# Kernel tuning notes

Measured on AMD Instinct MI355X. Metric: run time of the kernel, lower is better.

Reference implementation:

```python
import jax, jax.numpy as jnp
import numpy as np

L1, L2, B = 512, 512, 2
D1, D2, BN = 256, 256, 256
NEG = jnp.float32(-1e12)


def setup_inputs() -> dict:
    key = jax.random.key(0)
    ks = jax.random.split(key, 8)
    s = 0.05
    return {
        "ctx_1": jax.random.normal(ks[0], (L1, B, D1), jnp.float32),
        "ctx_2": jax.random.normal(ks[1], (L2, B, D2), jnp.float32),
        "ctx_1_mask": jnp.ones((L1, B), jnp.float32),
        "ctx_2_mask": jnp.ones((L2, B), jnp.float32),
        # mlp_hid: Conv2d(D1+D2 -> BN, 1x1) with bias
        "Wh": jax.random.normal(ks[2], (D1 + D2, BN), jnp.float32) * s,
        "bh": jnp.zeros((BN,), jnp.float32),
        # mlp_out: Conv2d(BN -> 1, 1x1), bias=False (mlp_bias default)
        "wo": jax.random.normal(ks[3], (BN,), jnp.float32) * s,
        # project_1_to_2 / project_2_to_1: Linear(D1+D2 -> BN) with bias
        "W12": jax.random.normal(ks[4], (D2 + D1, BN), jnp.float32) * s,
        "b12": jnp.zeros((BN,), jnp.float32),
        "W21": jax.random.normal(ks[5], (D1 + D2, BN), jnp.float32) * s,
        "b21": jnp.zeros((BN,), jnp.float32),
    }


def reference(ctx_1, ctx_2, ctx_1_mask, ctx_2_mask, Wh, bh, wo, W12, b12, W21, b21):
    d1 = ctx_1.shape[-1]
    # 1x1 conv on cat([b_ctx_1, b_ctx_2]) == sum of two independent projections
    Wh1, Wh2 = Wh[:d1], Wh[d1:]
    p1 = jnp.einsum('lbd,dk->blk', ctx_1, Wh1)            # (B, L1, K)
    p2 = jnp.einsum('mbd,dk->bmk', ctx_2, Wh2)            # (B, L2, K)
    hidden = jnp.tanh(p1[:, :, None, :] + p2[:, None, :, :] + bh)  # (B, L1, L2, K)
    affinity = jnp.einsum('blmk,k->blm', hidden, wo)      # (B, L1, L2)
    # masked in both directions
    affinity = affinity + (1.0 - ctx_1_mask.T)[:, :, None] * NEG
    affinity = affinity + (1.0 - ctx_2_mask.T)[:, None, :] * NEG
    # 1 -> 2 direction: softmax over L2
    dist_1_to_2 = jax.nn.softmax(affinity, axis=2)        # (B, L1, L2)
    context_1_to_2 = jnp.einsum('lbd,blm->mbd', ctx_1, dist_1_to_2)  # (L2, B, D1)
    seq_1_to_2 = jnp.tanh(jnp.concatenate([ctx_2, context_1_to_2], axis=-1) @ W12 + b12)
    # 2 -> 1 direction: softmax over L1 (then contracted over L2, as in the torch code)
    dist_2_to_1 = jax.nn.softmax(affinity, axis=1)        # (B, L1, L2)
    context_2_to_1 = jnp.einsum('mbd,blm->lbd', ctx_2, dist_2_to_1)  # (L1, B, D2)
    seq_2_to_1 = jnp.tanh(jnp.concatenate([ctx_1, context_2_to_1], axis=-1) @ W21 + b21)
    return (seq_2_to_1, seq_1_to_2)
```

## Files before the change

### kernel.cpp

```cpp
#include <hip/hip_runtime.h>


#define NEGC (-1e12f)
#define TWO_LOG2E 2.8853900817779268f
#define LOG2E 1.4426950408889634f
#define N2LOG2E (-2.8853900817779268f)

typedef __attribute__((ext_vector_type(8))) short bf16x8;
typedef __attribute__((ext_vector_type(4))) float f32x4;

__device__ __forceinline__ short f2bf(float x)
{
    union { float f; unsigned u; } v; v.f = x;
    unsigned r = (v.u + 0x7FFFu + ((v.u >> 16) & 1u)) >> 16;
    return (short)r;
}

__global__ __launch_bounds__(256) void k_projE(
    const float* __restrict__ ctx1, const float* __restrict__ ctx2,
    const float* __restrict__ Wh, const float* __restrict__ bh,
    const float* __restrict__ mask1, const float* __restrict__ mask2,
    float* __restrict__ E1, float* __restrict__ E2,
    float* __restrict__ p1, float* __restrict__ p2,
    float* __restrict__ S1, float* __restrict__ S2)
{
    const int t  = threadIdx.x;
    const int g  = blockIdx.z;
    const int r0 = blockIdx.x * 32;
    const int n0 = blockIdx.y * 64;

    const float* A    = g ? ctx2       : ctx1;
    const float* W    = g ? Wh + 65536 : Wh;
    const float* bias = g ? 0          : bh;
    float*       outp = g ? E2         : E1;

    if (g == 0 && blockIdx.x == 0 && blockIdx.y == 0) {
        for (int idx = t; idx < 1024; idx += 256) {
            int row = idx >> 1, b = idx & 1;
            p1[b * 512 + row] = __builtin_amdgcn_exp2f(LOG2E * (1.f - mask1[idx]) * NEGC);
            p2[b * 512 + row] = __builtin_amdgcn_exp2f(LOG2E * (1.f - mask2[idx]) * NEGC);
            S1[b * 512 + row] = 0.f;
            S2[b * 512 + row] = 0.f;
        }
    }

    __shared__ __align__(16) short Abf[32 * 264];
    __shared__ __align__(16) short Bbf[64 * 264];

    #pragma unroll
    for (int i = 0; i < 8; ++i) {
        int slot = i * 256 + t;
        int r = slot >> 6, kq = (slot & 63) << 2;
        float4 v = *(const float4*)(A + (r0 + r) * 256 + kq);
        short4 s; s.x = f2bf(v.x); s.y = f2bf(v.y); s.z = f2bf(v.z); s.w = f2bf(v.w);
        *(short4*)(Abf + r * 264 + kq) = s;
    }
    #pragma unroll
    for (int i = 0; i < 16; ++i) {
        int slot = i * 256 + t;
        int bk = slot >> 4, bn4 = (slot & 15) << 2;
        float4 v = *(const float4*)(W + bk * 256 + n0 + bn4);
        Bbf[(bn4 + 0) * 264 + bk] = f2bf(v.x);
        Bbf[(bn4 + 1) * 264 + bk] = f2bf(v.y);
        Bbf[(bn4 + 2) * 264 + bk] = f2bf(v.z);
        Bbf[(bn4 + 3) * 264 + bk] = f2bf(v.w);
    }
    __syncthreads();

    const int w    = t >> 6;
    const int lane = t & 63;
    const int quad = lane >> 4;
    const int lr   = lane & 15;
    const int h    = w & 1;
    const int c    = w >> 1;

    f32x4 acc[2] = {};

    #pragma unroll
    for (int s = 0; s < 8; ++s) {
        const int kb = s * 32 + quad * 8;
        bf16x8 a = *(const bf16x8*)(Abf + (h * 16 + lr) * 264 + kb);
        #pragma unroll
        for (int nc = 0; nc < 2; ++nc) {
            bf16x8 b = *(const bf16x8*)(Bbf + (c * 32 + nc * 16 + lr) * 264 + kb);
            acc[nc] = __builtin_amdgcn_mfma_f32_16x16x32_bf16(a, b, acc[nc], 0, 0, 0);
        }
    }

    #pragma unroll
    for (int nc = 0; nc < 2; ++nc) {
        const int col = n0 + c * 32 + nc * 16 + lr;
        const float bv = bias ? bias[col] : 0.f;
        #pragma unroll
        for (int reg = 0; reg < 4; ++reg) {
            int row  = r0 + h * 16 + quad * 4 + reg;
            int orow = ((row & 1) << 9) + (row >> 1);
            float v = acc[nc][reg] + bv;
            outp[orow * 256 + col] = __builtin_amdgcn_exp2f(v * TWO_LOG2E);
        }
    }
}

#define PAIR(AV, QV, WV, ACC) do {                                    \
    float x0_ = fmaf(AV.x, QV.x, 1.f);                                \
    float x1_ = fmaf(AV.y, QV.y, 1.f);                                \
    float x2_ = fmaf(AV.z, QV.z, 1.f);                                \
    float x3_ = fmaf(AV.w, QV.w, 1.f);                                \
    float r01_ = __builtin_amdgcn_rcpf(x0_ * x1_);                    \
    float r23_ = __builtin_amdgcn_rcpf(x2_ * x3_);                    \
    float z01_ = fmaf(WV.y, x0_, WV.x * x1_);                         \
    float z23_ = fmaf(WV.w, x2_, WV.z * x3_);                         \
    ACC = fmaf(r01_, z01_, ACC);                                      \
    ACC = fmaf(r23_, z23_, ACC);                                      \
} while (0)

__global__ __launch_bounds__(256) void k_mid(
    const float* __restrict__ ctx1, const float* __restrict__ ctx2,
    const float* __restrict__ W12, const float* __restrict__ b12,
    const float* __restrict__ W21, const float* __restrict__ b21,
    const float* __restrict__ E1g, const float* __restrict__ E2g,
    const float* __restrict__ wo,
    const float* __restrict__ p1g, const float* __restrict__ p2g,
    float* __restrict__ P12, float* __restrict__ U1,
    float* __restrict__ P21, float* __restrict__ U2,
    float* __restrict__ EN, float* __restrict__ ET,
    float* __restrict__ S1, float* __restrict__ S2)
{
    __shared__ __align__(16) char smem[38400];

    const int t   = threadIdx.x;
    const int bid = blockIdx.x;
    const int r3  = bid % 3;

    if (r3 == 2) {
        const int idx = bid / 3;
        const int g   = idx >> 6;
        const int r0  = (idx & 15) * 64;
        const int n0  = ((idx >> 4) & 3) * 64;

        const float* A; const float* W; const float* bias; float* outp;
        switch (g) {
          case 0:  A = ctx2; W = W12;         bias = b12; outp = P12; break;
          case 1:  A = ctx1; W = W12 + 65536; bias = 0;   outp = U1;  break;
          case 2:  A = ctx1; W = W21;         bias = b21; outp = P21; break;
          default: A = ctx2; W = W21 + 65536; bias = 0;   outp = U2;  break;
        }

        short* Abf = (short*)smem;
        short* Bbf = Abf + 64 * 136;

        const int w    = t >> 6;
        const int lane = t & 63;
        const int quad = lane >> 4;
        const int lr   = lane & 15;

        f32x4 acc[4] = {};

        for (int kc = 0; kc < 256; kc += 128) {
            #pragma unroll
            for (int i = 0; i < 8; ++i) {
                int slot = i * 256 + t;
                int r = slot >> 5, kq = (slot & 31) << 2;
                float4 v = *(const float4*)(A + (r0 + r) * 256 + kc + kq);
                short4 s; s.x = f2bf(v.x); s.y = f2bf(v.y); s.z = f2bf(v.z); s.w = f2bf(v.w);
                *(short4*)(Abf + r * 136 + kq) = s;
            }
            #pragma unroll
            for (int i = 0; i < 8; ++i) {
                int slot = i * 256 + t;
                int bk = slot >> 4, bn4 = (slot & 15) << 2;
                float4 v = *(const float4*)(W + (kc + bk) * 256 + n0 + bn4);
                Bbf[(bn4 + 0) * 136 + bk] = f2bf(v.x);
                Bbf[(bn4 + 1) * 136 + bk] = f2bf(v.y);
                Bbf[(bn4 + 2) * 136 + bk] = f2bf(v.z);
                Bbf[(bn4 + 3) * 136 + bk] = f2bf(v.w);
            }
            __syncthreads();
            #pragma unroll
            for (int s = 0; s < 4; ++s) {
                const int kb = s * 32 + quad * 8;
                bf16x8 a = *(const bf16x8*)(Abf + (w * 16 + lr) * 136 + kb);
                #pragma unroll
                for (int nc = 0; nc < 4; ++nc) {
                    bf16x8 b = *(const bf16x8*)(Bbf + (nc * 16 + lr) * 136 + kb);
                    acc[nc] = __builtin_amdgcn_mfma_f32_16x16x32_bf16(a, b, acc[nc], 0, 0, 0);
                }
            }
            __syncthreads();
        }

        #pragma unroll
        for (int nc = 0; nc < 4; ++nc) {
            const int col = n0 + nc * 16 + lr;
            const float bv = bias ? bias[col] : 0.f;
            #pragma unroll
            for (int reg = 0; reg < 4; ++reg) {
                int row  = r0 + w * 16 + quad * 4 + reg;
                int orow = ((row & 1) << 9) + (row >> 1);
                outp[orow * 256 + col] = acc[nc][reg] + bv;
            }
        }
    } else {
        const int aidx = (bid / 3) * 2 + r3;
        const int l0 = (aidx & 15) * 32;
        const int m0 = ((aidx >> 4) & 15) * 32;
        const int b  = aidx >> 8;

        float* E1s  = (float*)smem;
        float* E2s  = E1s + 32 * 132;
        float* affs = E2s + 32 * 132;

        const int tl = t >> 4, tm = t & 15;
        float acc[2][2] = {};

        for (int kc = 0; kc < 256; kc += 128) {
            #pragma unroll
            for (int i = 0; i < 4; ++i) {
                int slot = i * 256 + t;
                int r = slot >> 5, kq = (slot & 31) << 2;
                *(float4*)(E1s + r * 132 + kq) =
                    *(const float4*)(E1g + (((b << 9) + l0 + r) << 8) + kc + kq);
                *(float4*)(E2s + r * 132 + kq) =
                    *(const float4*)(E2g + (((b << 9) + m0 + r) << 8) + kc + kq);
            }
            __syncthreads();
            #pragma unroll 4
            for (int k0 = 0; k0 < 128; k0 += 4) {
                const float4 w  = *(const float4*)(wo + kc + k0);
                const float4 a0 = *(const float4*)(E1s + tl * 132 + k0);
                const float4 a1 = *(const float4*)(E1s + (tl + 16) * 132 + k0);
                const float4 q0 = *(const float4*)(E2s + tm * 132 + k0);
                const float4 q1 = *(const float4*)(E2s + (tm + 16) * 132 + k0);
                PAIR(a0, q0, w, acc[0][0]);
                PAIR(a0, q1, w, acc[0][1]);
                PAIR(a1, q0, w, acc[1][0]);
                PAIR(a1, q1, w, acc[1][1]);
            }
            __syncthreads();
        }

        affs[tl * 36 + tm]             = __builtin_amdgcn_exp2f(acc[0][0] * N2LOG2E);
        affs[tl * 36 + tm + 16]        = __builtin_amdgcn_exp2f(acc[0][1] * N2LOG2E);
        affs[(tl + 16) * 36 + tm]      = __builtin_amdgcn_exp2f(acc[1][0] * N2LOG2E);
        affs[(tl + 16) * 36 + tm + 16] = __builtin_amdgcn_exp2f(acc[1][1] * N2LOG2E);
        __syncthreads();

        const int r  = t >> 3;
        const int c4 = (t & 7) << 2;
        {
            float4 e = *(const float4*)(affs + r * 36 + c4);
            const float p1r = p1g[(b << 9) + l0 + r];
            float4 vn = make_float4(e.x * p1r, e.y * p1r, e.z * p1r, e.w * p1r);
            *(float4*)(EN + (((b << 9) + l0 + r) << 9) + m0 + c4) = vn;
            float4 p2v = *(const float4*)(p2g + (b << 9) + m0 + c4);
            float s = (e.x * p2v.x + e.y * p2v.y) + (e.z * p2v.z + e.w * p2v.w);
            s += __shfl_xor(s, 1, 64);
            s += __shfl_xor(s, 2, 64);
            s += __shfl_xor(s, 4, 64);
            if ((t & 7) == 0) atomicAdd(S1 + (b << 9) + l0 + r, s);
        }
        {
            float4 te;
            te.x = affs[(c4 + 0) * 36 + r];
            te.y = affs[(c4 + 1) * 36 + r];
            te.z = affs[(c4 + 2) * 36 + r];
            te.w = affs[(c4 + 3) * 36 + r];
            const float p2r = p2g[(b << 9) + m0 + r];
            float4 vt = make_float4(te.x * p2r, te.y * p2r, te.z * p2r, te.w * p2r);
            *(float4*)(ET + (((b << 9) + m0 + r) << 9) + l0 + c4) = vt;
            float4 p1v = *(const float4*)(p1g + (b << 9) + l0 + c4);
            float s = (te.x * p1v.x + te.y * p1v.y) + (te.z * p1v.z + te.w * p1v.w);
            s += __shfl_xor(s, 1, 64);
            s += __shfl_xor(s, 2, 64);
            s += __shfl_xor(s, 4, 64);
            if ((t & 7) == 0) atomicAdd(S2 + (b << 9) + m0 + r, s);
        }
    }
}

__global__ __launch_bounds__(256) void k_final(
    const float* __restrict__ EN, const float* __restrict__ ET,
    const float* __restrict__ U1, const float* __restrict__ U2,
    const float* __restrict__ P12, const float* __restrict__ P21,
    const float* __restrict__ S1, const float* __restrict__ S2,
    float* __restrict__ out)
{
    const int t   = threadIdx.x;
    const int r0  = blockIdx.x * 32, n0 = blockIdx.y * 32;
    const int dir = blockIdx.z >> 1, b = blockIdx.z & 1;
    const float* Ag = (dir == 0 ? ET  : EN)  + b * 262144;
    const float* Sg = (dir == 0 ? S1  : S2)  + b * 512;
    const float* Bg = (dir == 0 ? U1  : U2)  + b * 131072;
    const float* Pg = (dir == 0 ? P12 : P21) + b * 131072;
    float* o = out + (dir == 0 ? 262144 : 0);

    __shared__ __align__(16) short Abf[32 * 136];
    __shared__ __align__(16) short Bbf[32 * 136];
    __shared__ __align__(16) float rs[512];

    for (int i = t; i < 512; i += 256)
        rs[i] = __builtin_amdgcn_rcpf(Sg[i]);

    const int w    = t >> 6;
    const int lane = t & 63;
    const int quad = lane >> 4;
    const int lr   = lane & 15;
    const int wr   = (w >> 1) << 4, wc = (w & 1) << 4;
    const int col  = n0 + wc + lr;

    float pre[4];
    #pragma unroll
    for (int reg = 0; reg < 4; ++reg) {
        const int m = r0 + wr + quad * 4 + reg;
        pre[reg] = Pg[(m << 8) + col];
    }
    __syncthreads();

    f32x4 acc = {};

    for (int kc = 0; kc < 512; kc += 128) {
        #pragma unroll
        for (int i = 0; i < 4; ++i) {
            int slot = i * 256 + t;
            int r = slot >> 5, kq = (slot & 31) << 2;
            float4 v = *(const float4*)(Ag + ((r0 + r) << 9) + kc + kq);
            const float* rp = rs + kc + kq;
            short4 s;
            s.x = f2bf(v.x * rp[0]); s.y = f2bf(v.y * rp[1]);
            s.z = f2bf(v.z * rp[2]); s.w = f2bf(v.w * rp[3]);
            *(short4*)(Abf + r * 136 + kq) = s;
        }
        #pragma unroll
        for (int i = 0; i < 4; ++i) {
            int slot = i * 256 + t;
            int bk = slot >> 3, bn4 = (slot & 7) << 2;
            float4 v = *(const float4*)(Bg + ((kc + bk) << 8) + n0 + bn4);
            Bbf[(bn4 + 0) * 136 + bk] = f2bf(v.x);
            Bbf[(bn4 + 1) * 136 + bk] = f2bf(v.y);
            Bbf[(bn4 + 2) * 136 + bk] = f2bf(v.z);
            Bbf[(bn4 + 3) * 136 + bk] = f2bf(v.w);
        }
        __syncthreads();
        #pragma unroll
        for (int s = 0; s < 4; ++s) {
            const int kb = s * 32 + quad * 8;
            bf16x8 a  = *(const bf16x8*)(Abf + (wr + lr) * 136 + kb);
            bf16x8 bb = *(const bf16x8*)(Bbf + (wc + lr) * 136 + kb);
            acc = __builtin_amdgcn_mfma_f32_16x16x32_bf16(a, bb, acc, 0, 0, 0);
        }
        __syncthreads();
    }

    #pragma unroll
    for (int reg = 0; reg < 4; ++reg) {
        const int m = r0 + wr + quad * 4 + reg;
        float v = acc[reg] + pre[reg];
        float tv = 1.f - 2.f * __builtin_amdgcn_rcpf(
                       __builtin_amdgcn_exp2f(v * TWO_LOG2E) + 1.f);
        o[((m << 1) + b) * 256 + col] = tv;
    }
}

extern "C" void kernel_launch(void* const* d_in, const int* in_sizes, int n_in,
                              void* d_out, int out_size, void* d_ws, size_t ws_size,
                              hipStream_t stream)
{
    const float* ctx1 = (const float*)d_in[0];
    const float* ctx2 = (const float*)d_in[1];
    const float* m1   = (const float*)d_in[2];
    const float* m2   = (const float*)d_in[3];
    const float* Wh   = (const float*)d_in[4];
    const float* bh   = (const float*)d_in[5];
    const float* wo   = (const float*)d_in[6];
    const float* W12  = (const float*)d_in[7];
    const float* b12  = (const float*)d_in[8];
    const float* W21  = (const float*)d_in[9];
    const float* b21  = (const float*)d_in[10];
    float* out = (float*)d_out;
    float* ws  = (float*)d_ws;

    float* E1  = ws;
    float* E2  = E1  + 262144;
    float* P12 = E2  + 262144;
    float* U1  = P12 + 262144;
    float* P21 = U1  + 262144;
    float* U2  = P21 + 262144;
    float* p1  = U2  + 262144;
    float* p2  = p1  + 1024;
    float* S1  = p2  + 1024;
    float* S2  = S1  + 1024;
    float* EN  = S2  + 1024;
    float* ET  = EN  + 524288;

    hipLaunchKernelGGL(k_projE, dim3(32, 4, 2), dim3(256), 0, stream,
                       ctx1, ctx2, Wh, bh, m1, m2, E1, E2, p1, p2, S1, S2);
    hipLaunchKernelGGL(k_mid, dim3(768, 1, 1), dim3(256), 0, stream,
                       ctx1, ctx2, W12, b12, W21, b21,
                       E1, E2, wo, p1, p2,
                       P12, U1, P21, U2, EN, ET, S1, S2);
    hipLaunchKernelGGL(k_final, dim3(16, 8, 4), dim3(256), 0, stream,
                       EN, ET, U1, U2, P12, P21, S1, S2, out);
}
```

Before: 115.3 us.

## Regroup kernels: fuse all projections, split affinity into its own full-K kernel

Moves the W12/W21 projection GEMMs out of the mid kernel and runs them alongside the Wh projection in one launch. The affinity computation becomes a dedicated kernel that stages the full K=256 of E1/E2 in shared memory in a single pass, which removes one sync round. Its inner loop uses packed v_pk_fma_f32 via inline asm, and bf16 conversion now goes through the native __bf16 cast. The aim is to balance work across launches and cut per-block overhead, at the cost of higher LDS use per affinity block (about 71KB), which lowers occupancy.

After: 118.7 us. +3.0%, slower.

```diff
diff --git a/kernel.cpp b/kernel.cpp
--- a/kernel.cpp
+++ b/kernel.cpp
@@ -8,135 +8,120 @@
 
 typedef __attribute__((ext_vector_type(8))) short bf16x8;
 typedef __attribute__((ext_vector_type(4))) float f32x4;
+typedef __attribute__((ext_vector_type(2))) float f32x2;
 
 __device__ __forceinline__ short f2bf(float x)
 {
-    union { float f; unsigned u; } v; v.f = x;
-    unsigned r = (v.u + 0x7FFFu + ((v.u >> 16) & 1u)) >> 16;
-    return (short)r;
-}
-
-__global__ __launch_bounds__(256) void k_projE(
+    return __builtin_bit_cast(short, (__bf16)x);
+}
+
+__device__ __forceinline__ f32x2 pk_fma(f32x2 a, f32x2 b, f32x2 c)
+{
+    f32x2 d;
+    asm("v_pk_fma_f32 %0, %1, %2, %3" : "=v"(d) : "v"(a), "v"(b), "v"(c));
+    return d;
+}
+
+__global__ __launch_bounds__(256) void k_proj(
     const float* __restrict__ ctx1, const float* __restrict__ ctx2,
     const float* __restrict__ Wh, const float* __restrict__ bh,
+    const float* __restrict__ W12, const float* __restrict__ b12,
+    const float* __restrict__ W21, const float* __restrict__ b21,
     const float* __restrict__ mask1, const float* __restrict__ mask2,
     float* __restrict__ E1, float* __restrict__ E2,
+    float* __restrict__ P12, float* __restrict__ U1,
+    float* __restrict__ P21, float* __restrict__ U2,
     float* __restrict__ p1, float* __restrict__ p2,
     float* __restrict__ S1, float* __restrict__ S2)
 {
-    const int t  = threadIdx.x;
-    const int g  = blockIdx.z;
-    const int r0 = blockIdx.x * 32;
-    const int n0 = blockIdx.y * 64;
-
-    const float* A    = g ? ctx2       : ctx1;
-    const float* W    = g ? Wh + 65536 : Wh;
-    const float* bias = g ? 0          : bh;
-    float*       outp = g ? E2         : E1;
-
-    if (g == 0 && blockIdx.x == 0 && blockIdx.y == 0) {
-        for (int idx = t; idx < 1024; idx += 256) {
-            int row = idx >> 1, b = idx & 1;
-            p1[b * 512 + row] = __builtin_amdgcn_exp2f(LOG2E * (1.f - mask1[idx]) * NEGC);
-            p2[b * 512 + row] = __builtin_amdgcn_exp2f(LOG2E * (1.f - mask2[idx]) * NEGC);
-            S1[b * 512 + row] = 0.f;
-            S2[b * 512 + row] = 0.f;
-        }
-    }
-
-    __shared__ __align__(16) short Abf[32 * 264];
-    __shared__ __align__(16) short Bbf[64 * 264];
-
-    #pragma unroll
-    for (int i = 0; i < 8; ++i) {
-        int slot = i * 256 + t;
-        int r = slot >> 6, kq = (slot & 63) << 2;
-        float4 v = *(const float4*)(A + (r0 + r) * 256 + kq);
-        short4 s; s.x = f2bf(v.x); s.y = f2bf(v.y); s.z = f2bf(v.z); s.w = f2bf(v.w);
-        *(short4*)(Abf + r * 264 + kq) = s;
-    }
-    #pragma unroll
-    for (int i = 0; i < 16; ++i) {
-        int slot = i * 256 + t;
-        int bk = slot >> 4, bn4 = (slot & 15) << 2;
-        float4 v = *(const float4*)(W + bk * 256 + n0 + bn4);
-        Bbf[(bn4 + 0) * 264 + bk] = f2bf(v.x);
-        Bbf[(bn4 + 1) * 264 + bk] = f2bf(v.y);
-        Bbf[(bn4 + 2) * 264 + bk] = f2bf(v.z);
-        Bbf[(bn4 + 3) * 264 + bk] = f2bf(v.w);
-    }
-    __syncthreads();
+    __shared__ __align__(16) char smem[50688];
+
+    const int t    = threadIdx.x;
+    const int bid  = blockIdx.x;
+    const int path = bid & 1;
+    const int idx  = bid >> 1;
 
     const int w    = t >> 6;
     const int lane = t & 63;
     const int quad = lane >> 4;
     const int lr   = lane & 15;
-    const int h    = w & 1;
-    const int c    = w >> 1;
-
-    f32x4 acc[2] = {};
-
-    #pragma unroll
-    for (int s = 0; s < 8; ++s) {
-        const int kb = s * 32 + quad * 8;
-        bf16x8 a = *(const bf16x8*)(Abf + (h * 16 + lr) * 264 + kb);
+
+    if (bid == 0) {
+        for (int i = t; i < 1024; i += 256) {
+            int row = i >> 1, b = i & 1;
+            p1[b * 512 + row] = __builtin_amdgcn_exp2f(LOG2E * (1.f - mask1[i]) * NEGC);
+            p2[b * 512 + row] = __builtin_amdgcn_exp2f(LOG2E * (1.f - mask2[i]) * NEGC);
+            S1[b * 512 + row] = 0.f;
+            S2[b * 512 + row] = 0.f;
+        }
+    }
+
+    if (path == 0) {
+        const int g  = idx >> 7;
+        const int i7 = idx & 127;
+        const int r0 = (i7 & 31) * 32;
+        const int n0 = (i7 >> 5) * 64;
+
+        const float* A    = g ? ctx2       : ctx1;
+        const float* W    = g ? Wh + 65536 : Wh;
+        const float* bias = g ? 0          : bh;
+        float*       outp = g ? E2         : E1;
+
+        short* Abf = (short*)smem;
+        short* Bbf = Abf + 32 * 264;
+
+        #pragma unroll
+        for (int i = 0; i < 8; ++i) {
+            int slot = i * 256 + t;
+            int r = slot >> 6, kq = (slot & 63) << 2;
+            float4 v = *(const float4*)(A + (r0 + r) * 256 + kq);
+            short4 s; s.x = f2bf(v.x); s.y = f2bf(v.y); s.z = f2bf(v.z); s.w = f2bf(v.w);
+            *(short4*)(Abf + r * 264 + kq) = s;
+        }
+        #pragma unroll
+        for (int i = 0; i < 16; ++i) {
+            int slot = i * 256 + t;
+            int bk = slot >> 4, bn4 = (slot & 15) << 2;
+            float4 v = *(const float4*)(W + bk * 256 + n0 + bn4);
+            Bbf[(bn4 + 0) * 264 + bk] = f2bf(v.x);
+            Bbf[(bn4 + 1) * 264 + bk] = f2bf(v.y);
+            Bbf[(bn4 + 2) * 264 + bk] = f2bf(v.z);
+            Bbf[(bn4 + 3) * 264 + bk] = f2bf(v.w);
+        }
+        __syncthreads();
+
+        const int h = w & 1;
+        const int c = w >> 1;
+
+        f32x4 acc[2] = {};
+
+        #pragma unroll
+        for (int s = 0; s < 8; ++s) {
+            const int kb = s * 32 + quad * 8;
+            bf16x8 a = *(const bf16x8*)(Abf + (h * 16 + lr) * 264 + kb);
+            #pragma unroll
+            for (int nc = 0; nc < 2; ++nc) {
+                bf16x8 b = *(const bf16x8*)(Bbf + (c * 32 + nc * 16 + lr) * 264 + kb);
+                acc[nc] = __builtin_amdgcn_mfma_f32_16x16x32_bf16(a, b, acc[nc], 0, 0, 0);
+            }
+        }
+
         #pragma unroll
         for (int nc = 0; nc < 2; ++nc) {
-            bf16x8 b = *(const bf16x8*)(Bbf + (c * 32 + nc * 16 + lr) * 264 + kb);
-            acc[nc] = __builtin_amdgcn_mfma_f32_16x16x32_bf16(a, b, acc[nc], 0, 0, 0);
-        }
-    }
-
-    #pragma unroll
-    for (int nc = 0; nc < 2; ++nc) {
-        const int col = n0 + c * 32 + nc * 16 + lr;
-        const float bv = bias ? bias[col] : 0.f;
-        #pragma unroll
-        for (int reg = 0; reg < 4; ++reg) {
-            int row  = r0 + h * 16 + quad * 4 + reg;
-            int orow = ((row & 1) << 9) + (row >> 1);
-            float v = acc[nc][reg] + bv;
-            outp[orow * 256 + col] = __builtin_amdgcn_exp2f(v * TWO_LOG2E);
-        }
-    }
-}
-
-#define PAIR(AV, QV, WV, ACC) do {                                    \
-    float x0_ = fmaf(AV.x, QV.x, 1.f);                                \
-    float x1_ = fmaf(AV.y, QV.y, 1.f);                                \
-    float x2_ = fmaf(AV.z, QV.z, 1.f);                                \
-    float x3_ = fmaf(AV.w, QV.w, 1.f);                                \
-    float r01_ = __builtin_amdgcn_rcpf(x0_ * x1_);                    \
-    float r23_ = __builtin_amdgcn_rcpf(x2_ * x3_);                    \
-    float z01_ = fmaf(WV.y, x0_, WV.x * x1_);                         \
-    float z23_ = fmaf(WV.w, x2_, WV.z * x3_);                         \
-    ACC = fmaf(r01_, z01_, ACC);                                      \
-    ACC = fmaf(r23_, z23_, ACC);                                      \
-} while (0)
-
-__global__ __launch_bounds__(256) void k_mid(
-    const float* __restrict__ ctx1, const float* __restrict__ ctx2,
-    const float* __restrict__ W12, const float* __restrict__ b12,
-    const float* __restrict__ W21, const float* __restrict__ b21,
-    const float* __restrict__ E1g, const float* __restrict__ E2g,
-    const float* __restrict__ wo,
-    const float* __restrict__ p1g, const float* __restrict__ p2g,
-    float* __restrict__ P12, float* __restrict__ U1,
-    float* __restrict__ P21, float* __restrict__ U2,
-    float* __restrict__ EN, float* __restrict__ ET,
-    float* __restrict__ S1, float* __restrict__ S2)
-{
-    __shared__ __align__(16) char smem[38400];
-
-    const int t   = threadIdx.x;
-    const int bid = blockIdx.x;
-    const int r3  = bid % 3;
-
-    if (r3 == 2) {
-        const int idx = bid / 3;
-        const int g   = idx >> 6;
-        const int r0  = (idx & 15) * 64;
-        const int n0  = ((idx >> 4) & 3) * 64;
+            const int col = n0 + c * 32 + nc * 16 + lr;
+            const float bv = bias ? bias[col] : 0.f;
+            #pragma unroll
+            for (int reg = 0; reg < 4; ++reg) {
+                int row  = r0 + h * 16 + quad * 4 + reg;
+                int orow = ((row & 1) << 9) + (row >> 1);
+                float v = acc[nc][reg] + bv;
+                outp[orow * 256 + col] = __builtin_amdgcn_exp2f(v * TWO_LOG2E);
+            }
+        }
+    } else {
+        const int g  = idx >> 6;
+        const int r0 = (idx & 15) * 64;
+        const int n0 = ((idx >> 4) & 3) * 64;
 
         const float* A; const float* W; const float* bias; float* outp;
         switch (g) {
@@ -148,11 +133,6 @@
 
         short* Abf = (short*)smem;
         short* Bbf = Abf + 64 * 136;
-
-        const int w    = t >> 6;
-        const int lane = t & 63;
-        const int quad = lane >> 4;
-        const int lr   = lane & 15;
 
         f32x4 acc[4] = {};
 
@@ -200,81 +180,106 @@
                 outp[orow * 256 + col] = acc[nc][reg] + bv;
             }
         }
-    } else {
-        const int aidx = (bid / 3) * 2 + r3;
-        const int l0 = (aidx & 15) * 32;
-        const int m0 = ((aidx >> 4) & 15) * 32;
-        const int b  = aidx >> 8;
-
-        float* E1s  = (float*)smem;
-        float* E2s  = E1s + 32 * 132;
-        float* affs = E2s + 32 * 132;
-
-        const int tl = t >> 4, tm = t & 15;
-        float acc[2][2] = {};
-
-        for (int kc = 0; kc < 256; kc += 128) {
-            #pragma unroll
-            for (int i = 0; i < 4; ++i) {
-                int slot = i * 256 + t;
-                int r = slot >> 5, kq = (slot & 31) << 2;
-                *(float4*)(E1s + r * 132 + kq) =
-                    *(const float4*)(E1g + (((b << 9) + l0 + r) << 8) + kc + kq);
-                *(float4*)(E2s + r * 132 + kq) =
-                    *(const float4*)(E2g + (((b << 9) + m0 + r) << 8) + kc + kq);
-            }
-            __syncthreads();
-            #pragma unroll 4
-            for (int k0 = 0; k0 < 128; k0 += 4) {
-                const float4 w  = *(const float4*)(wo + kc + k0);
-                const float4 a0 = *(const float4*)(E1s + tl * 132 + k0);
-                const float4 a1 = *(const float4*)(E1s + (tl + 16) * 132 + k0);
-                const float4 q0 = *(const float4*)(E2s + tm * 132 + k0);
-                const float4 q1 = *(const float4*)(E2s + (tm + 16) * 132 + k0);
-                PAIR(a0, q0, w, acc[0][0]);
-                PAIR(a0, q1, w, acc[0][1]);
-                PAIR(a1, q0, w, acc[1][0]);
-                PAIR(a1, q1, w, acc[1][1]);
-            }
-            __syncthreads();
-        }
-
-        affs[tl * 36 + tm]             = __builtin_amdgcn_exp2f(acc[0][0] * N2LOG2E);
-        affs[tl * 36 + tm + 16]        = __builtin_amdgcn_exp2f(acc[0][1] * N2LOG2E);
-        affs[(tl + 16) * 36 + tm]      = __builtin_amdgcn_exp2f(acc[1][0] * N2LOG2E);
-        affs[(tl + 16) * 36 + tm + 16] = __builtin_amdgcn_exp2f(acc[1][1] * N2LOG2E);
-        __syncthreads();
-
-        const int r  = t >> 3;
-        const int c4 = (t & 7) << 2;
-        {
-            float4 e = *(const float4*)(affs + r * 36 + c4);
-            const float p1r = p1g[(b << 9) + l0 + r];
-            float4 vn = make_float4(e.x * p1r, e.y * p1r, e.z * p1r, e.w * p1r);
-            *(float4*)(EN + (((b << 9) + l0 + r) << 9) + m0 + c4) = vn;
-            float4 p2v = *(const float4*)(p2g + (b << 9) + m0 + c4);
-            float s = (e.x * p2v.x + e.y * p2v.y) + (e.z * p2v.z + e.w * p2v.w);
-            s += __shfl_xor(s, 1, 64);
-            s += __shfl_xor(s, 2, 64);
-            s += __shfl_xor(s, 4, 64);
-            if ((t & 7) == 0) atomicAdd(S1 + (b << 9) + l0 + r, s);
-        }
-        {
-            float4 te;
-            te.x = affs[(c4 + 0) * 36 + r];
-            te.y = affs[(c4 + 1) * 36 + r];
-            te.z = affs[(c4 + 2) * 36 + r];
-            te.w = affs[(c4 + 3) * 36 + r];
-            const float p2r = p2g[(b << 9) + m0 + r];
-            float4 vt = make_float4(te.x * p2r, te.y * p2r, te.z * p2r, te.w * p2r);
-            *(float4*)(ET + (((b << 9) + m0 + r) << 9) + l0 + c4) = vt;
-            float4 p1v = *(const float4*)(p1g + (b << 9) + l0 + c4);
-            float s = (te.x * p1v.x + te.y * p1v.y) + (te.z * p1v.z + te.w * p1v.w);
-            s += __shfl_xor(s, 1, 64);
-            s += __shfl_xor(s, 2, 64);
-            s += __shfl_xor(s, 4, 64);
-            if ((t & 7) == 0) atomicAdd(S2 + (b << 9) + m0 + r, s);
-        }
+    }
+}
+
+__device__ __forceinline__ void pair4(const float4 AV, const float4 QV,
+                                      const float4 WV, const f32x2 one,
+                                      float& ACC)
+{
+    f32x2 alo = {AV.x, AV.y}, ahi = {AV.z, AV.w};
+    f32x2 qlo = {QV.x, QV.y}, qhi = {QV.z, QV.w};
+    f32x2 x01 = pk_fma(alo, qlo, one);
+    f32x2 x23 = pk_fma(ahi, qhi, one);
+    float r01 = __builtin_amdgcn_rcpf(x01.x * x01.y);
+    float r23 = __builtin_amdgcn_rcpf(x23.x * x23.y);
+    float z01 = fmaf(WV.y, x01.x, WV.x * x01.y);
+    float z23 = fmaf(WV.w, x23.x, WV.z * x23.y);
+    ACC = fmaf(r01, z01, ACC);
+    ACC = fmaf(r23, z23, ACC);
+}
+
+__global__ __launch_bounds__(256) void k_aff(
+    const float* __restrict__ E1g, const float* __restrict__ E2g,
+    const float* __restrict__ wo,
+    const float* __restrict__ p1g, const float* __restrict__ p2g,
+    float* __restrict__ EN, float* __restrict__ ET,
+    float* __restrict__ S1, float* __restrict__ S2)
+{
+    const int t   = threadIdx.x;
+    const int bid = blockIdx.x;
+    const int l0 = (bid & 15) * 32;
+    const int m0 = ((bid >> 4) & 15) * 32;
+    const int b  = bid >> 8;
+
+    __shared__ __align__(16) float E1s[32 * 260];
+    __shared__ __align__(16) float E2s[32 * 260];
+    __shared__ __align__(16) float affs[32 * 36];
+
+    #pragma unroll
+    for (int i = 0; i < 8; ++i) {
+        int slot = i * 256 + t;
+        int r = slot >> 6, kq = (slot & 63) << 2;
+        *(float4*)(E1s + r * 260 + kq) =
+            *(const float4*)(E1g + (((b << 9) + l0 + r) << 8) + kq);
+        *(float4*)(E2s + r * 260 + kq) =
+            *(const float4*)(E2g + (((b << 9) + m0 + r) << 8) + kq);
+    }
+    __syncthreads();
+
+    const int tl = t >> 4, tm = t & 15;
+    float acc[2][2] = {};
+    const f32x2 one = {1.f, 1.f};
+
+    #pragma unroll 4
+    for (int k0 = 0; k0 < 256; k0 += 4) {
+        const float4 w  = *(const float4*)(wo + k0);
+        const float4 a0 = *(const float4*)(E1s + tl * 260 + k0);
+        const float4 a1 = *(const float4*)(E1s + (tl + 16) * 260 + k0);
+        const float4 q0 = *(const float4*)(E2s + tm * 260 + k0);
+        const float4 q1 = *(const float4*)(E2s + (tm + 16) * 260 + k0);
+        pair4(a0, q0, w, one, acc[0][0]);
+        pair4(a0, q1, w, one, acc[0][1]);
+        pair4(a1, q0, w, one, acc[1][0]);
+        pair4(a1, q1, w, one, acc[1][1]);
+    }
+    __syncthreads();
+
+    affs[tl * 36 + tm]             = __builtin_amdgcn_exp2f(acc[0][0] * N2LOG2E);
+    affs[tl * 36 + tm + 16]        = __builtin_amdgcn_exp2f(acc[0][1] * N2LOG2E);
+    affs[(tl + 16) * 36 + tm]      = __builtin_amdgcn_exp2f(acc[1][0] * N2LOG2E);
+    affs[(tl + 16) * 36 + tm + 16] = __builtin_amdgcn_exp2f(acc[1][1] * N2LOG2E);
+    __syncthreads();
+
+    const int r  = t >> 3;
+    const int c4 = (t & 7) << 2;
+    {
+        float4 e = *(const float4*)(affs + r * 36 + c4);
+        const float p1r = p1g[(b << 9) + l0 + r];
+        float4 vn = make_float4(e.x * p1r, e.y * p1r, e.z * p1r, e.w * p1r);
+        *(float4*)(EN + (((b << 9) + l0 + r) << 9) + m0 + c4) = vn;
+        float4 p2v = *(const float4*)(p2g + (b << 9) + m0 + c4);
+        float s = (e.x * p2v.x + e.y * p2v.y) + (e.z * p2v.z + e.w * p2v.w);
+        s += __shfl_xor(s, 1, 64);
+        s += __shfl_xor(s, 2, 64);
+        s += __shfl_xor(s, 4, 64);
+        if ((t & 7) == 0) atomicAdd(S1 + (b << 9) + l0 + r, s);
+    }
+    {
+        float4 te;
+        te.x = affs[(c4 + 0) * 36 + r];
+        te.y = affs[(c4 + 1) * 36 + r];
+        te.z = affs[(c4 + 2) * 36 + r];
+        te.w = affs[(c4 + 3) * 36 + r];
+        const float p2r = p2g[(b << 9) + m0 + r];
+        float4 vt = make_float4(te.x * p2r, te.y * p2r, te.z * p2r, te.w * p2r);
+        *(float4*)(ET + (((b << 9) + m0 + r) << 9) + l0 + c4) = vt;
+        float4 p1v = *(const float4*)(p1g + (b << 9) + l0 + c4);
+        float s = (te.x * p1v.x + te.y * p1v.y) + (te.z * p1v.z + te.w * p1v.w);
+        s += __shfl_xor(s, 1, 64);
+        s += __shfl_xor(s, 2, 64);
+        s += __shfl_xor(s, 4, 64);
+        if ((t & 7) == 0) atomicAdd(S2 + (b << 9) + m0 + r, s);
     }
 }
 
@@ -323,11 +328,11 @@
         for (int i = 0; i < 4; ++i) {
             int slot = i * 256 + t;
             int r = slot >> 5, kq = (slot & 31) << 2;
-            float4 v = *(const float4*)(Ag + ((r0 + r) << 9) + kc + kq);
-            const float* rp = rs + kc + kq;
+            float4 v  = *(const float4*)(Ag + ((r0 + r) << 9) + kc + kq);
+            float4 rv = *(const float4*)(rs + kc + kq);
             short4 s;
-            s.x = f2bf(v.x * rp[0]); s.y = f2bf(v.y * rp[1]);
-            s.z = f2bf(v.z * rp[2]); s.w = f2bf(v.w * rp[3]);
+            s.x = f2bf(v.x * rv.x); s.y = f2bf(v.y * rv.y);
+            s.z = f2bf(v.z * rv.z); s.w = f2bf(v.w * rv.w);
             *(short4*)(Abf + r * 136 + kq) = s;
         }
         #pragma unroll
@@ -392,12 +397,11 @@
     float* EN  = S2  + 1024;
     float* ET  = EN  + 524288;
 
-    hipLaunchKernelGGL(k_projE, dim3(32, 4, 2), dim3(256), 0, stream,
-                       ctx1, ctx2, Wh, bh, m1, m2, E1, E2, p1, p2, S1, S2);
-    hipLaunchKernelGGL(k_mid, dim3(768, 1, 1), dim3(256), 0, stream,
-                       ctx1, ctx2, W12, b12, W21, b21,
-                       E1, E2, wo, p1, p2,
-                       P12, U1, P21, U2, EN, ET, S1, S2);
+    hipLaunchKernelGGL(k_proj, dim3(512, 1, 1), dim3(256), 0, stream,
+                       ctx1, ctx2, Wh, bh, W12, b12, W21, b21, m1, m2,
+                       E1, E2, P12, U1, P21, U2, p1, p2, S1, S2);
+    hipLaunchKernelGGL(k_aff, dim3(512, 1, 1), dim3(256), 0, stream,
+                       E1, E2, wo, p1, p2, EN, ET, S1, S2);
     hipLaunchKernelGGL(k_final, dim3(16, 8, 4), dim3(256), 0, stream,
                        EN, ET, U1, U2, P12, P21, S1, S2, out);
 }
```

## Store affinity matrices as bf16 and fold softmax normalizer into B operand

Applied to the files above, without the earlier changes.

The mid kernel now writes the scaled affinity matrices EN/ET as bf16 rather than fp32, which halves the intermediate write and read traffic between kernels. The final kernel copies these bf16 tiles directly into shared memory with 16-byte loads. The per-k reciprocal softmax normalizer is now applied to the B operand (U1/U2) during its conversion, since the scale runs along the shared k dimension. The bf16 conversion now uses the compiler's native __bf16 cast. Risk: the normalization is now applied after bf16 rounding of the A values instead of before, which slightly changes rounding.

After: 113.3 us. Within noise of the previous version (-1.7%).

```diff
diff --git a/kernel.cpp b/kernel.cpp
--- a/kernel.cpp
+++ b/kernel.cpp
@@ -11,9 +11,7 @@
 
 __device__ __forceinline__ short f2bf(float x)
 {
-    union { float f; unsigned u; } v; v.f = x;
-    unsigned r = (v.u + 0x7FFFu + ((v.u >> 16) & 1u)) >> 16;
-    return (short)r;
+    return __builtin_bit_cast(short, (__bf16)x);
 }
 
 __global__ __launch_bounds__(256) void k_projE(
@@ -123,7 +121,7 @@
     const float* __restrict__ p1g, const float* __restrict__ p2g,
     float* __restrict__ P12, float* __restrict__ U1,
     float* __restrict__ P21, float* __restrict__ U2,
-    float* __restrict__ EN, float* __restrict__ ET,
+    short* __restrict__ EN, short* __restrict__ ET,
     float* __restrict__ S1, float* __restrict__ S2)
 {
     __shared__ __align__(16) char smem[38400];
@@ -250,8 +248,10 @@
         {
             float4 e = *(const float4*)(affs + r * 36 + c4);
             const float p1r = p1g[(b << 9) + l0 + r];
-            float4 vn = make_float4(e.x * p1r, e.y * p1r, e.z * p1r, e.w * p1r);
-            *(float4*)(EN + (((b << 9) + l0 + r) << 9) + m0 + c4) = vn;
+            short4 vn;
+            vn.x = f2bf(e.x * p1r); vn.y = f2bf(e.y * p1r);
+            vn.z = f2bf(e.z * p1r); vn.w = f2bf(e.w * p1r);
+            *(short4*)(EN + (((b << 9) + l0 + r) << 9) + m0 + c4) = vn;
             float4 p2v = *(const float4*)(p2g + (b << 9) + m0 + c4);
             float s = (e.x * p2v.x + e.y * p2v.y) + (e.z * p2v.z + e.w * p2v.w);
             s += __shfl_xor(s, 1, 64);
@@ -266,8 +266,10 @@
             te.z = affs[(c4 + 2) * 36 + r];
             te.w = affs[(c4 + 3) * 36 + r];
             const float p2r = p2g[(b << 9) + m0 + r];
-            float4 vt = make_float4(te.x * p2r, te.y * p2r, te.z * p2r, te.w * p2r);
-            *(float4*)(ET + (((b << 9) + m0 + r) << 9) + l0 + c4) = vt;
+            short4 vt;
+            vt.x = f2bf(te.x * p2r); vt.y = f2bf(te.y * p2r);
+            vt.z = f2bf(te.z * p2r); vt.w = f2bf(te.w * p2r);
+            *(short4*)(ET + (((b << 9) + m0 + r) << 9) + l0 + c4) = vt;
             float4 p1v = *(const float4*)(p1g + (b << 9) + l0 + c4);
             float s = (te.x * p1v.x + te.y * p1v.y) + (te.z * p1v.z + te.w * p1v.w);
             s += __shfl_xor(s, 1, 64);
@@ -279,7 +281,7 @@
 }
 
 __global__ __launch_bounds__(256) void k_final(
-    const float* __restrict__ EN, const float* __restrict__ ET,
+    const short* __restrict__ EN, const short* __restrict__ ET,
     const float* __restrict__ U1, const float* __restrict__ U2,
     const float* __restrict__ P12, const float* __restrict__ P21,
     const float* __restrict__ S1, const float* __restrict__ S2,
@@ -288,7 +290,7 @@
     const int t   = threadIdx.x;
     const int r0  = blockIdx.x * 32, n0 = blockIdx.y * 32;
     const int dir = blockIdx.z >> 1, b = blockIdx.z & 1;
-    const float* Ag = (dir == 0 ? ET  : EN)  + b * 262144;
+    const short* Ag = (dir == 0 ? ET  : EN)  + b * 262144;
     const float* Sg = (dir == 0 ? S1  : S2)  + b * 512;
     const float* Bg = (dir == 0 ? U1  : U2)  + b * 131072;
     const float* Pg = (dir == 0 ? P12 : P21) + b * 131072;
@@ -320,25 +322,22 @@
 
     for (int kc = 0; kc < 512; kc += 128) {
         #pragma unroll
-        for (int i = 0; i < 4; ++i) {
+        for (int i = 0; i < 2; ++i) {
             int slot = i * 256 + t;
-            int r = slot >> 5, kq = (slot & 31) << 2;
-            float4 v = *(const float4*)(Ag + ((r0 + r) << 9) + kc + kq);
-            const float* rp = rs + kc + kq;
-            short4 s;
-            s.x = f2bf(v.x * rp[0]); s.y = f2bf(v.y * rp[1]);
-            s.z = f2bf(v.z * rp[2]); s.w = f2bf(v.w * rp[3]);
-            *(short4*)(Abf + r * 136 + kq) = s;
+            int r = slot >> 4, k8 = (slot & 15) << 3;
+            *(bf16x8*)(Abf + r * 136 + k8) =
+                *(const bf16x8*)(Ag + ((r0 + r) << 9) + kc + k8);
         }
         #pragma unroll
         for (int i = 0; i < 4; ++i) {
             int slot = i * 256 + t;
             int bk = slot >> 3, bn4 = (slot & 7) << 2;
             float4 v = *(const float4*)(Bg + ((kc + bk) << 8) + n0 + bn4);
-            Bbf[(bn4 + 0) * 136 + bk] = f2bf(v.x);
-            Bbf[(bn4 + 1) * 136 + bk] = f2bf(v.y);
-            Bbf[(bn4 + 2) * 136 + bk] = f2bf(v.z);
-            Bbf[(bn4 + 3) * 136 + bk] = f2bf(v.w);
+            const float rsv = rs[kc + bk];
+            Bbf[(bn4 + 0) * 136 + bk] = f2bf(v.x * rsv);
+            Bbf[(bn4 + 1) * 136 + bk] = f2bf(v.y * rsv);
+            Bbf[(bn4 + 2) * 136 + bk] = f2bf(v.z * rsv);
+            Bbf[(bn4 + 3) * 136 + bk] = f2bf(v.w * rsv);
         }
         __syncthreads();
         #pragma unroll
@@ -389,15 +388,17 @@
     float* p2  = p1  + 1024;
     float* S1  = p2  + 1024;
     float* S2  = S1  + 1024;
-    float* EN  = S2  + 1024;
-    float* ET  = EN  + 524288;
+    float* ENf = S2  + 1024;
+    float* ETf = ENf + 524288;
+    short* EN16 = (short*)ENf;
+    short* ET16 = (short*)ETf;
 
     hipLaunchKernelGGL(k_projE, dim3(32, 4, 2), dim3(256), 0, stream,
                        ctx1, ctx2, Wh, bh, m1, m2, E1, E2, p1, p2, S1, S2);
     hipLaunchKernelGGL(k_mid, dim3(768, 1, 1), dim3(256), 0, stream,
                        ctx1, ctx2, W12, b12, W21, b21,
                        E1, E2, wo, p1, p2,
-                       P12, U1, P21, U2, EN, ET, S1, S2);
+                       P12, U1, P21, U2, EN16, ET16, S1, S2);
     hipLaunchKernelGGL(k_final, dim3(16, 8, 4), dim3(256), 0, stream,
-                       EN, ET, U1, U2, P12, P21, S1, S2, out);
+                       EN16, ET16, U1, U2, P12, P21, S1, S2, out);
 }
```
